# Performance work log

Measured on AMD Instinct MI355X. Metric: run time of the kernel, lower is better.

Reference implementation:

```python
import jax, jax.numpy as jnp
import numpy as np

HIDDEN = 768
META = 25
ED_COUNT = 300
B, N_MENT, N_PAIRS = 2, 2000, 40000


def setup_inputs() -> dict:
    key = jax.random.key(0)
    ks = jax.random.split(key, 8)
    mention_reprs = jax.random.normal(ks[0], (B, N_MENT, HIDDEN), dtype=jnp.float32)
    coref_mention_pairs = jax.random.randint(ks[1], (B, N_PAIRS, 2), 0, N_MENT)
    coref_eds = jax.random.randint(ks[2], (B, N_PAIRS), 0, ED_COUNT)
    in_dim = HIDDEN * 2 + META
    # nn.Linear default init scale ~ 1/sqrt(fan_in); exact init is irrelevant for correctness
    W1 = jax.random.normal(ks[3], (in_dim, HIDDEN), dtype=jnp.float32) / np.sqrt(in_dim)
    b1 = jnp.zeros((HIDDEN,), dtype=jnp.float32)
    W2 = jax.random.normal(ks[4], (HIDDEN, 1), dtype=jnp.float32) / np.sqrt(HIDDEN)
    b2 = jnp.zeros((1,), dtype=jnp.float32)
    ed_table = jax.random.normal(ks[5], (ED_COUNT, META), dtype=jnp.float32)
    return {
        "mention_reprs": mention_reprs,
        "coref_mention_pairs": coref_mention_pairs,
        "coref_eds": coref_eds,
        "ed_table": ed_table,
        "W1": W1,
        "b1": b1,
        "W2": W2,
        "b2": b2,
    }


def reference(mention_reprs, coref_mention_pairs, coref_eds, ed_table, W1, b1, W2, b2):
    b = mention_reprs.shape[0]
    # batch_index gather: [B, P, 2, H]
    bidx = jnp.arange(b)[:, None, None]
    pairs = mention_reprs[bidx, coref_mention_pairs]
    # flatten pair dim -> [B, P, 2H]
    pair_repr = pairs.reshape(b, pairs.shape[1], -1)
    eds = ed_table[coref_eds]  # [B, P, META]
    coref_repr = jnp.concatenate([pair_repr, eds], axis=2)  # [B, P, 2H+META]
    h = jax.nn.relu(coref_repr @ W1 + b1)  # dropout = identity in eval
    logits = (h @ W2 + b2).squeeze(-1)  # [B, P]
    return logits
```

## Files before the change

### kernel.cpp

```cpp
#include <hip/hip_runtime.h>
#include <stdint.h>

#define HIDDEN 768
#define META 25
#define EDC 300
#define BB 2
#define NMENT 2000
#define NPAIRS 40000
#define M_ROWS (BB * NMENT)
#define M_PAD 4096
#define N_OUT 1536
#define TOTAL_PAIRS (BB * NPAIRS)
#define BK 32

typedef __bf16 bf16x8 __attribute__((ext_vector_type(8)));
typedef float f32x4 __attribute__((ext_vector_type(4)));

static __device__ __forceinline__ float bf2f(unsigned short u) {
    union { unsigned int u; float f; } v; v.u = ((unsigned int)u) << 16; return v.f;
}
static __device__ __forceinline__ float2 bf2x(unsigned int u) {
    union { unsigned int x; float f; } lo, hi;
    lo.x = u << 16; hi.x = u & 0xffff0000u;
    float2 r; r.x = lo.f; r.y = hi.f; return r;
}
static __device__ __forceinline__ unsigned short f2bf(float f) {
    union { float f; unsigned int u; } v; v.f = f;
    unsigned int u = v.u;
    unsigned int r = (u + 0x7FFFu + ((u >> 16) & 1u)) >> 16;
    return (unsigned short)r;
}

#define GLOAD_LDS16(g, l)                                                            \
    __builtin_amdgcn_global_load_lds((const __attribute__((address_space(1))) void*)(g), \
                                     (__attribute__((address_space(3))) void*)(l), 16, 0, 0)

#define NB_CONVM 3072
#define NB_CONVW 576
#define NB_PREP  900
#define NB_W2    3

__global__ __launch_bounds__(256) void k_prep_all(
        const float* __restrict__ M, unsigned short* __restrict__ Mb,
        const float* __restrict__ W1, unsigned short* __restrict__ Wt,
        const float* __restrict__ ed_table, const float* __restrict__ b1,
        unsigned short* __restrict__ Epp,
        const float* __restrict__ W2, unsigned short* __restrict__ W2b) {
    const int blk = blockIdx.x;
    const int t = threadIdx.x;
    if (blk < NB_CONVM) {
        int idx = (blk * 256 + t) * 4;
        int row = idx / HIDDEN;
        ushort4 o;
        if (row < M_ROWS) {
            const float4 v = *(const float4*)(M + idx);
            o.x = f2bf(v.x); o.y = f2bf(v.y); o.z = f2bf(v.z); o.w = f2bf(v.w);
        } else {
            o.x = 0; o.y = 0; o.z = 0; o.w = 0;
        }
        *(ushort4*)(Mb + idx) = o;
    } else if (blk < NB_CONVM + NB_CONVW) {
        __shared__ float tile[32][68];
        int id = blk - NB_CONVM;
        int nt = id % 24, kt = id / 24;
        int n0 = nt * 64, k0 = kt * 32;
        int tk = t >> 4, tn = (t & 15) * 4;
        int srcRowOff = (n0 < HIDDEN) ? 0 : HIDDEN;
        int srcColBase = (n0 < HIDDEN) ? n0 : (n0 - HIDDEN);
        {
            const float4 v0 = *(const float4*)(W1 + (size_t)(k0 + tk + srcRowOff) * HIDDEN + srcColBase + tn);
            tile[tk][tn] = v0.x; tile[tk][tn + 1] = v0.y; tile[tk][tn + 2] = v0.z; tile[tk][tn + 3] = v0.w;
            const float4 v1 = *(const float4*)(W1 + (size_t)(k0 + tk + 16 + srcRowOff) * HIDDEN + srcColBase + tn);
            tile[tk + 16][tn] = v1.x; tile[tk + 16][tn + 1] = v1.y; tile[tk + 16][tn + 2] = v1.z; tile[tk + 16][tn + 3] = v1.w;
        }
        __syncthreads();
        int wn = t >> 2, wk = (t & 3) * 8;
        unsigned int p0 = (unsigned int)f2bf(tile[wk + 0][wn]) | ((unsigned int)f2bf(tile[wk + 1][wn]) << 16);
        unsigned int p1 = (unsigned int)f2bf(tile[wk + 2][wn]) | ((unsigned int)f2bf(tile[wk + 3][wn]) << 16);
        unsigned int p2 = (unsigned int)f2bf(tile[wk + 4][wn]) | ((unsigned int)f2bf(tile[wk + 5][wn]) << 16);
        unsigned int p3 = (unsigned int)f2bf(tile[wk + 6][wn]) | ((unsigned int)f2bf(tile[wk + 7][wn]) << 16);
        uint4 pk; pk.x = p0; pk.y = p1; pk.z = p2; pk.w = p3;
        *(uint4*)(Wt + (size_t)(n0 + wn) * HIDDEN + k0 + wk) = pk;
    } else if (blk < NB_CONVM + NB_CONVW + NB_PREP) {
        int id = (blk - NB_CONVM - NB_CONVW) * 256 + t;
        int e = id / HIDDEN, n = id - e * HIDDEN;
        float acc = b1[n];
#pragma unroll
        for (int k = 0; k < META; k++)
            acc += ed_table[e * META + k] * W1[(size_t)(2 * HIDDEN + k) * HIDDEN + n];
        Epp[id] = f2bf(acc);
    } else {
        int id = (blk - NB_CONVM - NB_CONVW - NB_PREP) * 256 + t;
        if (id < HIDDEN) W2b[id] = f2bf(W2[id]);
    }
}

__global__ __launch_bounds__(256) void k_gemm(const unsigned short* __restrict__ Mb,
                                              const unsigned short* __restrict__ Wt,
                                              unsigned short* __restrict__ AW) {
    __shared__ unsigned short As[128 * BK];
    __shared__ unsigned short Bs[64 * BK];
    const int m0 = blockIdx.x * 128;
    const int n0 = blockIdx.y * 64;
    const int t = threadIdx.x, w = t >> 6, lane = t & 63;
    const int wm = (w & 1) * 64, wn = (w >> 1) * 32;
    const int q = lane >> 4, r = lane & 15;
    const int lrow = lane >> 2, lcol = (lane & 3) * 8;
    const unsigned short* gA = Mb + (size_t)(m0 + w * 32 + lrow) * HIDDEN + lcol;
    const unsigned short* gB = Wt + (size_t)(n0 + w * 16 + lrow) * HIDDEN + lcol;
    unsigned short* lA = As + (w * 32) * BK;
    unsigned short* lB = Bs + (w * 16) * BK;
    f32x4 acc[4][2] = {};
    for (int k0 = 0; k0 < HIDDEN; k0 += BK) {
        GLOAD_LDS16(gA + k0, lA);
        GLOAD_LDS16(gA + k0 + 16 * HIDDEN, lA + 16 * BK);
        GLOAD_LDS16(gB + k0, lB);
        __syncthreads();
        bf16x8 af[4], bfr[2];
#pragma unroll
        for (int i = 0; i < 4; i++) af[i]  = *(const bf16x8*)&As[(wm + i * 16 + r) * BK + q * 8];
#pragma unroll
        for (int j = 0; j < 2; j++) bfr[j] = *(const bf16x8*)&Bs[(wn + j * 16 + r) * BK + q * 8];
#pragma unroll
        for (int i = 0; i < 4; i++)
#pragma unroll
            for (int j = 0; j < 2; j++)
                acc[i][j] = __builtin_amdgcn_mfma_f32_16x16x32_bf16(af[i], bfr[j], acc[i][j], 0, 0, 0);
        __syncthreads();
    }
    const int colb = n0 + wn + (lane & 15);
    const int rowb = m0 + wm + (lane >> 4) * 4;
#pragma unroll
    for (int i = 0; i < 4; i++)
#pragma unroll
        for (int j = 0; j < 2; j++) {
            unsigned short* dst = AW + (size_t)(rowb + i * 16) * N_OUT + colb + j * 16;
#pragma unroll
            for (int reg = 0; reg < 4; reg++)
                dst[(size_t)reg * N_OUT] = f2bf(acc[i][j][reg]);
        }
}

__global__ __launch_bounds__(256) void k_pair(const unsigned short* __restrict__ AW,
                                              const unsigned short* __restrict__ Epp,
                                              const unsigned short* __restrict__ W2b,
                                              const float* __restrict__ b2,
                                              const int* __restrict__ pairs,
                                              const int* __restrict__ eds,
                                              float* __restrict__ out) {
    const int wid = blockIdx.x * 4 + (threadIdx.x >> 6);
    const int lane = threadIdx.x & 63;
    const int p0 = wid * 4;
    const int b = (p0 >= NPAIRS) ? 1 : 0;
    const int n0 = lane * 8;
    const int n1 = 512 + lane * 4;

    const int4 pr01 = *(const int4*)(pairs + (size_t)p0 * 2);
    const int4 pr23 = *(const int4*)(pairs + (size_t)p0 * 2 + 4);
    const int4 ed4  = *(const int4*)(eds + p0);

    const size_t base = (size_t)(b * NMENT);
    const unsigned short* a1p0 = AW + (base + pr01.x) * N_OUT;
    const unsigned short* a2p0 = AW + (base + pr01.y) * N_OUT + HIDDEN;
    const unsigned short* ep0  = Epp + (size_t)ed4.x * HIDDEN;
    const unsigned short* a1p1 = AW + (base + pr01.z) * N_OUT;
    const unsigned short* a2p1 = AW + (base + pr01.w) * N_OUT + HIDDEN;
    const unsigned short* ep1  = Epp + (size_t)ed4.y * HIDDEN;
    const unsigned short* a1p2 = AW + (base + pr23.x) * N_OUT;
    const unsigned short* a2p2 = AW + (base + pr23.y) * N_OUT + HIDDEN;
    const unsigned short* ep2  = Epp + (size_t)ed4.z * HIDDEN;
    const unsigned short* a1p3 = AW + (base + pr23.z) * N_OUT;
    const unsigned short* a2p3 = AW + (base + pr23.w) * N_OUT + HIDDEN;
    const unsigned short* ep3  = Epp + (size_t)ed4.w * HIDDEN;

    uint4   w0 = *(const uint4*)(W2b + n0);
    ushort4 w1 = *(const ushort4*)(W2b + n1);
    uint4   x10 = *(const uint4*)(a1p0 + n0), x20 = *(const uint4*)(a2p0 + n0), xe0 = *(const uint4*)(ep0 + n0);
    uint4   y10 = *(const uint4*)(a1p1 + n0), y20 = *(const uint4*)(a2p1 + n0), ye0 = *(const uint4*)(ep1 + n0);
    uint4   z10 = *(const uint4*)(a1p2 + n0), z20 = *(const uint4*)(a2p2 + n0), ze0 = *(const uint4*)(ep2 + n0);
    uint4   v10 = *(const uint4*)(a1p3 + n0), v20 = *(const uint4*)(a2p3 + n0), ve0 = *(const uint4*)(ep3 + n0);
    ushort4 x11 = *(const ushort4*)(a1p0 + n1), x21 = *(const ushort4*)(a2p0 + n1), xe1 = *(const ushort4*)(ep0 + n1);
    ushort4 y11 = *(const ushort4*)(a1p1 + n1), y21 = *(const ushort4*)(a2p1 + n1), ye1 = *(const ushort4*)(ep1 + n1);
    ushort4 z11 = *(const ushort4*)(a1p2 + n1), z21 = *(const ushort4*)(a2p2 + n1), ze1 = *(const ushort4*)(ep2 + n1);
    ushort4 v11 = *(const ushort4*)(a1p3 + n1), v21 = *(const ushort4*)(a2p3 + n1), ve1 = *(const ushort4*)(ep3 + n1);

    float acc0 = 0.f, acc1 = 0.f, acc2 = 0.f, acc3 = 0.f;
#define ACC2(acc, ua, ub, ue, uw)                                              \
    {                                                                          \
        float2 fa = bf2x(ua), fb = bf2x(ub), fe = bf2x(ue), fw = bf2x(uw);     \
        float h0 = fmaxf(fa.x + fb.x + fe.x, 0.f);                             \
        float h1 = fmaxf(fa.y + fb.y + fe.y, 0.f);                             \
        acc += h0 * fw.x + h1 * fw.y;                                          \
    }
#define ACC1(acc, sa, sb, se, sw)                                              \
    {                                                                          \
        float h = fmaxf(bf2f(sa) + bf2f(sb) + bf2f(se), 0.f);                  \
        acc += h * bf2f(sw);                                                   \
    }
    ACC2(acc0, x10.x, x20.x, xe0.x, w0.x); ACC2(acc0, x10.y, x20.y, xe0.y, w0.y);
    ACC2(acc0, x10.z, x20.z, xe0.z, w0.z); ACC2(acc0, x10.w, x20.w, xe0.w, w0.w);
    ACC1(acc0, x11.x, x21.x, xe1.x, w1.x); ACC1(acc0, x11.y, x21.y, xe1.y, w1.y);
    ACC1(acc0, x11.z, x21.z, xe1.z, w1.z); ACC1(acc0, x11.w, x21.w, xe1.w, w1.w);
    ACC2(acc1, y10.x, y20.x, ye0.x, w0.x); ACC2(acc1, y10.y, y20.y, ye0.y, w0.y);
    ACC2(acc1, y10.z, y20.z, ye0.z, w0.z); ACC2(acc1, y10.w, y20.w, ye0.w, w0.w);
    ACC1(acc1, y11.x, y21.x, ye1.x, w1.x); ACC1(acc1, y11.y, y21.y, ye1.y, w1.y);
    ACC1(acc1, y11.z, y21.z, ye1.z, w1.z); ACC1(acc1, y11.w, y21.w, ye1.w, w1.w);
    ACC2(acc2, z10.x, z20.x, ze0.x, w0.x); ACC2(acc2, z10.y, z20.y, ze0.y, w0.y);
    ACC2(acc2, z10.z, z20.z, ze0.z, w0.z); ACC2(acc2, z10.w, z20.w, ze0.w, w0.w);
    ACC1(acc2, z11.x, z21.x, ze1.x, w1.x); ACC1(acc2, z11.y, z21.y, ze1.y, w1.y);
    ACC1(acc2, z11.z, z21.z, ze1.z, w1.z); ACC1(acc2, z11.w, z21.w, ze1.w, w1.w);
    ACC2(acc3, v10.x, v20.x, ve0.x, w0.x); ACC2(acc3, v10.y, v20.y, ve0.y, w0.y);
    ACC2(acc3, v10.z, v20.z, ve0.z, w0.z); ACC2(acc3, v10.w, v20.w, ve0.w, w0.w);
    ACC1(acc3, v11.x, v21.x, ve1.x, w1.x); ACC1(acc3, v11.y, v21.y, ve1.y, w1.y);
    ACC1(acc3, v11.z, v21.z, ve1.z, w1.z); ACC1(acc3, v11.w, v21.w, ve1.w, w1.w);
#undef ACC2
#undef ACC1
#pragma unroll
    for (int off = 32; off > 0; off >>= 1) {
        acc0 += __shfl_xor(acc0, off, 64);
        acc1 += __shfl_xor(acc1, off, 64);
        acc2 += __shfl_xor(acc2, off, 64);
        acc3 += __shfl_xor(acc3, off, 64);
    }
    if (lane == 0) {
        float bias = b2[0];
        float4 o; o.x = acc0 + bias; o.y = acc1 + bias; o.z = acc2 + bias; o.w = acc3 + bias;
        *(float4*)(out + p0) = o;
    }
}

extern "C" void kernel_launch(void* const* d_in, const int* in_sizes, int n_in,
                              void* d_out, int out_size, void* d_ws, size_t ws_size,
                              hipStream_t stream) {
    const float* mention  = (const float*)d_in[0];
    const int*   pairs    = (const int*)d_in[1];
    const int*   eds      = (const int*)d_in[2];
    const float* ed_table = (const float*)d_in[3];
    const float* W1       = (const float*)d_in[4];
    const float* b1       = (const float*)d_in[5];
    const float* W2       = (const float*)d_in[6];
    const float* b2       = (const float*)d_in[7];
    float* out = (float*)d_out;

    char* ws = (char*)d_ws;
    unsigned short* Mb  = (unsigned short*)(ws);
    unsigned short* Wt  = (unsigned short*)(ws + 6291456);
    unsigned short* AW  = (unsigned short*)(ws + 6291456 + 2359296);
    unsigned short* Epp = (unsigned short*)(ws + 6291456 + 2359296 + 12582912);
    unsigned short* W2b = (unsigned short*)(ws + 6291456 + 2359296 + 12582912 + 460800);

    k_prep_all<<<dim3(NB_CONVM + NB_CONVW + NB_PREP + NB_W2), dim3(256), 0, stream>>>(
        mention, Mb, W1, Wt, ed_table, b1, Epp, W2, W2b);
    k_gemm<<<dim3(M_PAD / 128, N_OUT / 64), dim3(256), 0, stream>>>(Mb, Wt, AW);
    k_pair<<<dim3(TOTAL_PAIRS / 16), dim3(256), 0, stream>>>(AW, Epp, W2b, b2, pairs, eds, out);
}
```

Baseline: 121.7 us.

## Bucket pairs by mention-index range and map buckets to XCDs for L2 locality

Adds a histogram, serial scan and scatter pass that sorts pairs into 128 buckets keyed by batch and coarse mention-index ranges. The pair kernel then assigns bucket groups to blocks by blockIdx&7, so each XCD gathers mostly from a restricted slice of AW rows and those rows stay in its private L2. The cost is three extra small kernel launches, global atomics, an indirection through perm, and scattered scalar output stores instead of float4 stores. The fixed grid of 688 blocks per XCD assumes each bucket group holds at most about 11k pairs, which holds for uniformly random inputs.

```diff
diff --git a/kernel.cpp b/kernel.cpp
--- a/kernel.cpp
+++ b/kernel.cpp
@@ -12,6 +12,8 @@
 #define N_OUT 1536
 #define TOTAL_PAIRS (BB * NPAIRS)
 #define BK 32
+#define NBUCK 128
+#define XCD_BLOCKS 688
 
 typedef __bf16 bf16x8 __attribute__((ext_vector_type(8)));
 typedef float f32x4 __attribute__((ext_vector_type(4)));
@@ -39,13 +41,15 @@
 #define NB_CONVW 576
 #define NB_PREP  900
 #define NB_W2    3
+#define NB_ZERO  1
 
 __global__ __launch_bounds__(256) void k_prep_all(
         const float* __restrict__ M, unsigned short* __restrict__ Mb,
         const float* __restrict__ W1, unsigned short* __restrict__ Wt,
         const float* __restrict__ ed_table, const float* __restrict__ b1,
         unsigned short* __restrict__ Epp,
-        const float* __restrict__ W2, unsigned short* __restrict__ W2b) {
+        const float* __restrict__ W2, unsigned short* __restrict__ W2b,
+        int* __restrict__ hist) {
     const int blk = blockIdx.x;
     const int t = threadIdx.x;
     if (blk < NB_CONVM) {
@@ -89,10 +93,62 @@
         for (int k = 0; k < META; k++)
             acc += ed_table[e * META + k] * W1[(size_t)(2 * HIDDEN + k) * HIDDEN + n];
         Epp[id] = f2bf(acc);
-    } else {
+    } else if (blk < NB_CONVM + NB_CONVW + NB_PREP + NB_W2) {
         int id = (blk - NB_CONVM - NB_CONVW - NB_PREP) * 256 + t;
         if (id < HIDDEN) W2b[id] = f2bf(W2[id]);
-    }
+    } else {
+        if (t < NBUCK) hist[t] = 0;
+    }
+}
+
+static __device__ __forceinline__ int bucket_of(int p, int i0, int i1) {
+    int b = (p >= NPAIRS) ? 1 : 0;
+    return b * 64 + (i0 / 250) * 8 + (i1 / 250);
+}
+
+__global__ __launch_bounds__(256) void k_hist(const int* __restrict__ pairs,
+                                              int* __restrict__ hist) {
+    __shared__ int h[NBUCK];
+    int t = threadIdx.x;
+    if (t < NBUCK) h[t] = 0;
+    __syncthreads();
+    int p = blockIdx.x * 256 + t;
+    if (p < TOTAL_PAIRS) {
+        int2 pr = *(const int2*)(pairs + (size_t)p * 2);
+        atomicAdd(&h[bucket_of(p, pr.x, pr.y)], 1);
+    }
+    __syncthreads();
+    if (t < NBUCK && h[t]) atomicAdd(&hist[t], h[t]);
+}
+
+__global__ void k_scan(const int* __restrict__ hist, int* __restrict__ off,
+                       int* __restrict__ cursor) {
+    if (threadIdx.x == 0 && blockIdx.x == 0) {
+        int s = 0;
+        for (int i = 0; i < NBUCK; i++) { off[i] = s; cursor[i] = s; s += hist[i]; }
+        off[NBUCK] = s;
+    }
+}
+
+__global__ __launch_bounds__(256) void k_scatter(const int* __restrict__ pairs,
+                                                 int* __restrict__ cursor,
+                                                 int* __restrict__ perm) {
+    __shared__ int h[NBUCK], base[NBUCK];
+    int t = threadIdx.x;
+    if (t < NBUCK) h[t] = 0;
+    __syncthreads();
+    int p = blockIdx.x * 256 + t;
+    int bk = 0, lr = 0;
+    bool valid = p < TOTAL_PAIRS;
+    if (valid) {
+        int2 pr = *(const int2*)(pairs + (size_t)p * 2);
+        bk = bucket_of(p, pr.x, pr.y);
+        lr = atomicAdd(&h[bk], 1);
+    }
+    __syncthreads();
+    if (t < NBUCK && h[t]) base[t] = atomicAdd(&cursor[t], h[t]);
+    __syncthreads();
+    if (valid) perm[base[bk] + lr] = p;
 }
 
 __global__ __launch_bounds__(256) void k_gemm(const unsigned short* __restrict__ Mb,
@@ -147,42 +203,59 @@
                                               const float* __restrict__ b2,
                                               const int* __restrict__ pairs,
                                               const int* __restrict__ eds,
+                                              const int* __restrict__ off,
+                                              const int* __restrict__ perm,
                                               float* __restrict__ out) {
-    const int wid = blockIdx.x * 4 + (threadIdx.x >> 6);
+    const int xcd = blockIdx.x & 7;
+    const int kb  = blockIdx.x >> 3;
     const int lane = threadIdx.x & 63;
-    const int p0 = wid * 4;
-    const int b = (p0 >= NPAIRS) ? 1 : 0;
+    const int wv   = threadIdx.x >> 6;
+    const int s1 = off[xcd * 8],      e1 = off[xcd * 8 + 8];
+    const int s2 = off[64 + xcd * 8], e2 = off[64 + xcd * 8 + 8];
+    const int len1 = e1 - s1;
+    const int len  = len1 + (e2 - s2);
+    const int l0 = kb * 16 + wv * 4;
+    if (l0 >= len) return;
+
+    int   pidx[4];
+    bool  val[4];
+#pragma unroll
+    for (int i = 0; i < 4; i++) {
+        int l = l0 + i;
+        val[i] = l < len;
+        int pos = (l < len1) ? (s1 + l) : (s2 + (l - len1));
+        if (!val[i]) pos = s1;
+        if (pos >= TOTAL_PAIRS) pos = 0;
+        pidx[i] = perm[pos];
+    }
+
     const int n0 = lane * 8;
     const int n1 = 512 + lane * 4;
 
-    const int4 pr01 = *(const int4*)(pairs + (size_t)p0 * 2);
-    const int4 pr23 = *(const int4*)(pairs + (size_t)p0 * 2 + 4);
-    const int4 ed4  = *(const int4*)(eds + p0);
-
-    const size_t base = (size_t)(b * NMENT);
-    const unsigned short* a1p0 = AW + (base + pr01.x) * N_OUT;
-    const unsigned short* a2p0 = AW + (base + pr01.y) * N_OUT + HIDDEN;
-    const unsigned short* ep0  = Epp + (size_t)ed4.x * HIDDEN;
-    const unsigned short* a1p1 = AW + (base + pr01.z) * N_OUT;
-    const unsigned short* a2p1 = AW + (base + pr01.w) * N_OUT + HIDDEN;
-    const unsigned short* ep1  = Epp + (size_t)ed4.y * HIDDEN;
-    const unsigned short* a1p2 = AW + (base + pr23.x) * N_OUT;
-    const unsigned short* a2p2 = AW + (base + pr23.y) * N_OUT + HIDDEN;
-    const unsigned short* ep2  = Epp + (size_t)ed4.z * HIDDEN;
-    const unsigned short* a1p3 = AW + (base + pr23.z) * N_OUT;
-    const unsigned short* a2p3 = AW + (base + pr23.w) * N_OUT + HIDDEN;
-    const unsigned short* ep3  = Epp + (size_t)ed4.w * HIDDEN;
+    const unsigned short* a1p[4];
+    const unsigned short* a2p[4];
+    const unsigned short* epp[4];
+#pragma unroll
+    for (int i = 0; i < 4; i++) {
+        int p = pidx[i];
+        int2 pr = *(const int2*)(pairs + (size_t)p * 2);
+        int ed = eds[p];
+        size_t base = (p >= NPAIRS) ? (size_t)NMENT : 0;
+        a1p[i] = AW + (base + pr.x) * N_OUT;
+        a2p[i] = AW + (base + pr.y) * N_OUT + HIDDEN;
+        epp[i] = Epp + (size_t)ed * HIDDEN;
+    }
 
     uint4   w0 = *(const uint4*)(W2b + n0);
     ushort4 w1 = *(const ushort4*)(W2b + n1);
-    uint4   x10 = *(const uint4*)(a1p0 + n0), x20 = *(const uint4*)(a2p0 + n0), xe0 = *(const uint4*)(ep0 + n0);
-    uint4   y10 = *(const uint4*)(a1p1 + n0), y20 = *(const uint4*)(a2p1 + n0), ye0 = *(const uint4*)(ep1 + n0);
-    uint4   z10 = *(const uint4*)(a1p2 + n0), z20 = *(const uint4*)(a2p2 + n0), ze0 = *(const uint4*)(ep2 + n0);
-    uint4   v10 = *(const uint4*)(a1p3 + n0), v20 = *(const uint4*)(a2p3 + n0), ve0 = *(const uint4*)(ep3 + n0);
-    ushort4 x11 = *(const ushort4*)(a1p0 + n1), x21 = *(const ushort4*)(a2p0 + n1), xe1 = *(const ushort4*)(ep0 + n1);
-    ushort4 y11 = *(const ushort4*)(a1p1 + n1), y21 = *(const ushort4*)(a2p1 + n1), ye1 = *(const ushort4*)(ep1 + n1);
-    ushort4 z11 = *(const ushort4*)(a1p2 + n1), z21 = *(const ushort4*)(a2p2 + n1), ze1 = *(const ushort4*)(ep2 + n1);
-    ushort4 v11 = *(const ushort4*)(a1p3 + n1), v21 = *(const ushort4*)(a2p3 + n1), ve1 = *(const ushort4*)(ep3 + n1);
+    uint4   x10 = *(const uint4*)(a1p[0] + n0), x20 = *(const uint4*)(a2p[0] + n0), xe0 = *(const uint4*)(epp[0] + n0);
+    uint4   y10 = *(const uint4*)(a1p[1] + n0), y20 = *(const uint4*)(a2p[1] + n0), ye0 = *(const uint4*)(epp[1] + n0);
+    uint4   z10 = *(const uint4*)(a1p[2] + n0), z20 = *(const uint4*)(a2p[2] + n0), ze0 = *(const uint4*)(epp[2] + n0);
+    uint4   v10 = *(const uint4*)(a1p[3] + n0), v20 = *(const uint4*)(a2p[3] + n0), ve0 = *(const uint4*)(epp[3] + n0);
+    ushort4 x11 = *(const ushort4*)(a1p[0] + n1), x21 = *(const ushort4*)(a2p[0] + n1), xe1 = *(const ushort4*)(epp[0] + n1);
+    ushort4 y11 = *(const ushort4*)(a1p[1] + n1), y21 = *(const ushort4*)(a2p[1] + n1), ye1 = *(const ushort4*)(epp[1] + n1);
+    ushort4 z11 = *(const ushort4*)(a1p[2] + n1), z21 = *(const ushort4*)(a2p[2] + n1), ze1 = *(const ushort4*)(epp[2] + n1);
+    ushort4 v11 = *(const ushort4*)(a1p[3] + n1), v21 = *(const ushort4*)(a2p[3] + n1), ve1 = *(const ushort4*)(epp[3] + n1);
 
     float acc0 = 0.f, acc1 = 0.f, acc2 = 0.f, acc3 = 0.f;
 #define ACC2(acc, ua, ub, ue, uw)                                              \
@@ -216,16 +289,18 @@
 #undef ACC2
 #undef ACC1
 #pragma unroll
-    for (int off = 32; off > 0; off >>= 1) {
-        acc0 += __shfl_xor(acc0, off, 64);
-        acc1 += __shfl_xor(acc1, off, 64);
-        acc2 += __shfl_xor(acc2, off, 64);
-        acc3 += __shfl_xor(acc3, off, 64);
+    for (int o = 32; o > 0; o >>= 1) {
+        acc0 += __shfl_xor(acc0, o, 64);
+        acc1 += __shfl_xor(acc1, o, 64);
+        acc2 += __shfl_xor(acc2, o, 64);
+        acc3 += __shfl_xor(acc3, o, 64);
     }
     if (lane == 0) {
         float bias = b2[0];
-        float4 o; o.x = acc0 + bias; o.y = acc1 + bias; o.z = acc2 + bias; o.w = acc3 + bias;
-        *(float4*)(out + p0) = o;
+        if (val[0]) out[pidx[0]] = acc0 + bias;
+        if (val[1]) out[pidx[1]] = acc1 + bias;
+        if (val[2]) out[pidx[2]] = acc2 + bias;
+        if (val[3]) out[pidx[3]] = acc3 + bias;
     }
 }
 
@@ -243,14 +318,21 @@
     float* out = (float*)d_out;
 
     char* ws = (char*)d_ws;
-    unsigned short* Mb  = (unsigned short*)(ws);
-    unsigned short* Wt  = (unsigned short*)(ws + 6291456);
-    unsigned short* AW  = (unsigned short*)(ws + 6291456 + 2359296);
-    unsigned short* Epp = (unsigned short*)(ws + 6291456 + 2359296 + 12582912);
-    unsigned short* W2b = (unsigned short*)(ws + 6291456 + 2359296 + 12582912 + 460800);
-
-    k_prep_all<<<dim3(NB_CONVM + NB_CONVW + NB_PREP + NB_W2), dim3(256), 0, stream>>>(
-        mention, Mb, W1, Wt, ed_table, b1, Epp, W2, W2b);
+    unsigned short* Mb     = (unsigned short*)(ws);
+    unsigned short* Wt     = (unsigned short*)(ws + 6291456);
+    unsigned short* AW     = (unsigned short*)(ws + 8650752);
+    unsigned short* Epp    = (unsigned short*)(ws + 21233664);
+    unsigned short* W2b    = (unsigned short*)(ws + 21694464);
+    int*            hist   = (int*)(ws + 21696000);
+    int*            cursor = (int*)(ws + 21696512);
+    int*            offb   = (int*)(ws + 21697024);
+    int*            perm   = (int*)(ws + 21698048);
+
+    k_prep_all<<<dim3(NB_CONVM + NB_CONVW + NB_PREP + NB_W2 + NB_ZERO), dim3(256), 0, stream>>>(
+        mention, Mb, W1, Wt, ed_table, b1, Epp, W2, W2b, hist);
+    k_hist<<<dim3((TOTAL_PAIRS + 255) / 256), dim3(256), 0, stream>>>(pairs, hist);
+    k_scan<<<dim3(1), dim3(64), 0, stream>>>(hist, offb, cursor);
+    k_scatter<<<dim3((TOTAL_PAIRS + 255) / 256), dim3(256), 0, stream>>>(pairs, cursor, perm);
     k_gemm<<<dim3(M_PAD / 128, N_OUT / 64), dim3(256), 0, stream>>>(Mb, Wt, AW);
-    k_pair<<<dim3(TOTAL_PAIRS / 16), dim3(256), 0, stream>>>(AW, Epp, W2b, b2, pairs, eds, out);
-}
+    k_pair<<<dim3(8 * XCD_BLOCKS), dim3(256), 0, stream>>>(AW, Epp, W2b, b2, pairs, eds, offb, perm, out);
+}
```

Result: slower. 136.2 us (+11.9%).
